# Performance work log

Measured on AMD Instinct MI355X. Metric: run time of the kernel, lower is better.

## Reference

```python
import jax, jax.numpy as jnp
import numpy as np

NEG_INF = -100000000.0  # matches masked_fill value in torch source

def setup_inputs() -> dict:
    key = jax.random.key(0)
    ks = jax.random.split(key, 7)
    d_model, d = 1024, 128
    B, S = 4, 2048
    scale = 1.0 / np.sqrt(d_model)
    x = jax.random.normal(ks[0], (B, S, d_model), dtype=jnp.float32)
    Wq = jax.random.normal(ks[1], (d, d_model), dtype=jnp.float32) * scale
    bq = jax.random.normal(ks[2], (d,), dtype=jnp.float32) * 0.02
    Wk = jax.random.normal(ks[3], (d, d_model), dtype=jnp.float32) * scale
    bk = jax.random.normal(ks[4], (d,), dtype=jnp.float32) * 0.02
    Wv = jax.random.normal(ks[5], (d, d_model), dtype=jnp.float32) * scale
    bv = jax.random.normal(ks[6], (d,), dtype=jnp.float32) * 0.02
    return {"x": x, "Wq": Wq, "bq": bq, "Wk": Wk, "bk": bk, "Wv": Wv, "bv": bv}

def reference(x, Wq, bq, Wk, bk, Wv, bv):
    # Q,K,V: [B,S,d] via torch Linear (x @ W.T + b)
    Q = jnp.einsum('bsm,dm->bsd', x, Wq) + bq
    K = jnp.einsum('bsm,dm->bsd', x, Wk) + bk
    V = jnp.einsum('bsm,dm->bsd', x, Wv) + bv
    d = Wk.shape[0]
    scale = 1.0 / jnp.sqrt(jnp.asarray(d, dtype=Q.dtype))
    scores = jnp.einsum('bqd,bkd->bqk', Q, K) * scale  # [B,S,S]
    # Faithful to source: tril then value-based mask (tril==0 -> -1e8).
    tril = jnp.tril(scores)
    masked = jnp.where(tril == 0, NEG_INF, tril)
    attn = jax.nn.softmax(masked, axis=-1)
    context = jnp.einsum('bqk,bkd->bqd', attn, V)
    return context
```

## Files before the change

### kernel.cpp

```cpp
#include <hip/hip_runtime.h>

typedef __attribute__((ext_vector_type(8))) short bf16x8;
typedef __attribute__((ext_vector_type(4))) float f32x4;

__device__ __forceinline__ unsigned short f2bf(float f) {
    unsigned int u = __float_as_uint(f);
    u += 0x7fffu + ((u >> 16) & 1u);
    return (unsigned short)(u >> 16);
}
__device__ __forceinline__ unsigned int pack2bf(float lo, float hi) {
    return (unsigned int)f2bf(lo) | ((unsigned int)f2bf(hi) << 16);
}
__device__ __forceinline__ void async_ld16(void* lds, const void* g) {
    __builtin_amdgcn_global_load_lds(
        (const __attribute__((address_space(1))) unsigned int*)g,
        (__attribute__((address_space(3))) unsigned int*)lds, 16, 0, 0);
}

__global__ __launch_bounds__(256) void conv_w(
    const float* __restrict__ Wq, const float* __restrict__ Wk,
    const float* __restrict__ Wv, unsigned short* __restrict__ Wcat)
{
    size_t o = ((size_t)blockIdx.x * 256 + threadIdx.x) * 8;
    int sel = (int)(o >> 17);
    const float* W = (sel == 0) ? Wq : ((sel == 1) ? Wk : Wv);
    const float* src = W + (o & 131071);
    float4 f0 = ((const float4*)src)[0];
    float4 f1 = ((const float4*)src)[1];
    uint4 u;
    u.x = pack2bf(f0.x, f0.y); u.y = pack2bf(f0.z, f0.w);
    u.z = pack2bf(f1.x, f1.y); u.w = pack2bf(f1.z, f1.w);
    *(uint4*)(Wcat + o) = u;
}

__global__ __launch_bounds__(256) void qkv_gemm(
    const float* __restrict__ x,
    const unsigned short* __restrict__ Wcat,
    const float* __restrict__ bq, const float* __restrict__ bk,
    const float* __restrict__ bv,
    unsigned short* __restrict__ Qg,
    unsigned short* __restrict__ Kg,
    unsigned short* __restrict__ Vtg)
{
    __shared__ unsigned short As[2][32 * 64];
    __shared__ unsigned short Bs[2][128 * 64];

    const int tid  = threadIdx.x;
    const int lane = tid & 63;
    const int w    = tid >> 6;
    const int quad = lane >> 4;
    const int ln   = lane & 15;
    const int lr   = lane >> 3;
    const int csw  = ((lane & 7) ^ lr) * 8;

    const int bid   = blockIdx.x;
    const int nb    = bid >> 8;
    const int mbase = (bid & 255) * 32;
    const unsigned short* Wsel = Wcat + (size_t)nb * 128 * 1024;

    const int arow  = tid >> 3;
    const int achk  = tid & 7;
    const int aslot = achk ^ (arow & 7);
    const float* xsrc = x + (size_t)(mbase + arow) * 1024 + achk * 8;
    unsigned short* adst0 = &As[0][arow * 64 + aslot * 8];
    unsigned short* adst1 = &As[1][arow * 64 + aslot * 8];

    f32x4 acc[2][2];
#pragma unroll
    for (int mt = 0; mt < 2; mt++)
#pragma unroll
        for (int nt = 0; nt < 2; nt++) acc[mt][nt] = (f32x4){0.f, 0.f, 0.f, 0.f};

    auto stageB = [&](int kb, int p) {
        const int kcol = kb * 64 + csw;
#pragma unroll
        for (int j = 0; j < 4; j++) {
            int chunk = w * 4 + j;
            async_ld16(&Bs[p][chunk * 512 + lane * 8],
                       Wsel + (size_t)(chunk * 8 + lr) * 1024 + kcol);
        }
    };
    auto writeA = [&](int p, const float4& f0, const float4& f1) {
        uint4 u;
        u.x = pack2bf(f0.x, f0.y); u.y = pack2bf(f0.z, f0.w);
        u.z = pack2bf(f1.x, f1.y); u.w = pack2bf(f1.z, f1.w);
        *(uint4*)((p == 0) ? adst0 : adst1) = u;
    };

    float4 a0 = ((const float4*)xsrc)[0];
    float4 a1 = ((const float4*)xsrc)[1];
    stageB(0, 0);
    writeA(0, a0, a1);
    __syncthreads();

    for (int kb = 0; kb < 16; kb++) {
        const int p = kb & 1;
        float4 n0, n1;
        if (kb < 15) {
            stageB(kb + 1, p ^ 1);
            const float* xs = xsrc + (kb + 1) * 64;
            n0 = ((const float4*)xs)[0];
            n1 = ((const float4*)xs)[1];
        }
#pragma unroll
        for (int ks = 0; ks < 2; ks++) {
            bf16x8 a[2], b[2];
#pragma unroll
            for (int mt = 0; mt < 2; mt++) {
                int row = mt * 16 + ln;
                a[mt] = *(const bf16x8*)&As[p][row * 64 + ((ks * 4 + quad) ^ (ln & 7)) * 8];
            }
#pragma unroll
            for (int nt = 0; nt < 2; nt++) {
                int row = w * 32 + nt * 16 + ln;
                b[nt] = *(const bf16x8*)&Bs[p][row * 64 + ((ks * 4 + quad) ^ (ln & 7)) * 8];
            }
#pragma unroll
            for (int mt = 0; mt < 2; mt++)
#pragma unroll
                for (int nt = 0; nt < 2; nt++)
                    acc[mt][nt] = __builtin_amdgcn_mfma_f32_16x16x32_bf16(
                        a[mt], b[nt], acc[mt][nt], 0, 0, 0);
        }
        if (kb < 15) writeA(p ^ 1, n0, n1);
        __syncthreads();
    }

    const float scale = (nb == 0) ? 0.08838834764831845f : 1.0f;
    const float* bsel = (nb == 0) ? bq : ((nb == 1) ? bk : bv);
    float bias_v[2];
#pragma unroll
    for (int nt = 0; nt < 2; nt++) bias_v[nt] = bsel[w * 32 + nt * 16 + ln];

    if (nb < 2) {
        unsigned short* dst = (nb == 0) ? Qg : Kg;
#pragma unroll
        for (int mt = 0; mt < 2; mt++)
#pragma unroll
            for (int nt = 0; nt < 2; nt++)
#pragma unroll
                for (int r = 0; r < 4; r++) {
                    int m = mbase + mt * 16 + quad * 4 + r;
                    int d = w * 32 + nt * 16 + ln;
                    dst[(size_t)m * 128 + d] =
                        f2bf((acc[mt][nt][r] + bias_v[nt]) * scale);
                }
    } else {
#pragma unroll
        for (int mt = 0; mt < 2; mt++)
#pragma unroll
            for (int nt = 0; nt < 2; nt++) {
                int dd = w * 32 + nt * 16 + ln;
                int m0 = mbase + mt * 16 + quad * 4;
                int bb = m0 >> 11, s0 = m0 & 2047;
                ushort4 u = { f2bf(acc[mt][nt][0] + bias_v[nt]),
                              f2bf(acc[mt][nt][1] + bias_v[nt]),
                              f2bf(acc[mt][nt][2] + bias_v[nt]),
                              f2bf(acc[mt][nt][3] + bias_v[nt]) };
                *(ushort4*)&Vtg[((size_t)bb * 128 + dd) * 2048 + s0] = u;
            }
    }
}

__global__ __launch_bounds__(256) void flash_attn(
    const unsigned short* __restrict__ Qg,
    const unsigned short* __restrict__ Kg,
    const unsigned short* __restrict__ Vtg,
    unsigned short* __restrict__ Opart,
    float2* __restrict__ ml)
{
    __shared__ unsigned short Ks[2][64 * 128];
    __shared__ unsigned short Vts[2][128 * 64];
    __shared__ unsigned short Pl[64][72];

    const int b = blockIdx.x;
    const int q = blockIdx.y;
    const int c = blockIdx.z;
    if (c > (q >> 2)) return;

    const int m4 = q >> 2, r4 = q & 3;
    const int pidx = b * 144 + q + 2 * m4 * (m4 - 1) + r4 * m4 + c;
    const int k0 = c * 4;
    const int kend = (c * 4 + 4 < q + 1) ? (c * 4 + 4) : (q + 1);

    const int tid  = threadIdx.x;
    const int lane = tid & 63, w = tid >> 6, quad = lane >> 4, ln = lane & 15;

    bf16x8 qa[4];
    const unsigned short* qrow =
        Qg + ((size_t)b * 2048 + q * 64 + w * 16 + ln) * 128 + quad * 8;
#pragma unroll
    for (int ks = 0; ks < 4; ks++) qa[ks] = *(const bf16x8*)(qrow + ks * 32);

    auto stage = [&](int kt, int p) {
        const unsigned short* ksrc = Kg + ((size_t)b * 2048 + kt * 64) * 128;
        const int krl = lane >> 4;
#pragma unroll
        for (int j = 0; j < 4; j++) {
            int chunk = w * 4 + j;
            int row = chunk * 4 + krl;
            int cd = (lane & 15) ^ (row & 15);
            async_ld16(&Ks[p][chunk * 512 + lane * 8],
                       ksrc + (size_t)row * 128 + cd * 8);
        }
        const unsigned short* vsrc = Vtg + (size_t)b * 128 * 2048 + kt * 64;
        const int vrl = lane >> 3;
#pragma unroll
        for (int j = 0; j < 4; j++) {
            int chunk = w * 4 + j;
            int row = chunk * 8 + vrl;
            int cd = (lane & 7) ^ (row & 7);
            async_ld16(&Vts[p][chunk * 512 + lane * 8],
                       vsrc + (size_t)row * 2048 + cd * 8);
        }
    };

    float m_i[4], l_i[4];
    f32x4 Ofr[8];
#pragma unroll
    for (int r = 0; r < 4; r++) { m_i[r] = -__builtin_inff(); l_i[r] = 0.f; }
#pragma unroll
    for (int dt = 0; dt < 8; dt++) Ofr[dt] = (f32x4){0.f, 0.f, 0.f, 0.f};

    stage(k0, 0);
    __syncthreads();

    int p = 0;
    for (int kt = k0; kt < kend; kt++) {
        if (kt + 1 < kend) stage(kt + 1, p ^ 1);

        f32x4 sfr[4];
#pragma unroll
        for (int ct = 0; ct < 4; ct++) {
            f32x4 s = (f32x4){0.f, 0.f, 0.f, 0.f};
#pragma unroll
            for (int ks = 0; ks < 4; ks++) {
                int row = ct * 16 + ln;
                bf16x8 kf = *(const bf16x8*)&Ks[p][row * 128 + ((ks * 4 + quad) ^ ln) * 8];
                s = __builtin_amdgcn_mfma_f32_16x16x32_bf16(qa[ks], kf, s, 0, 0, 0);
            }
            sfr[ct] = s;
        }

        if (kt == q) {
#pragma unroll
            for (int ct = 0; ct < 4; ct++)
#pragma unroll
                for (int r = 0; r < 4; r++)
                    if (ct * 16 + ln > w * 16 + quad * 4 + r)
                        sfr[ct][r] = -__builtin_inff();
        }

        float mrow[4];
#pragma unroll
        for (int r = 0; r < 4; r++) mrow[r] = -__builtin_inff();
#pragma unroll
        for (int ct = 0; ct < 4; ct++)
#pragma unroll
            for (int r = 0; r < 4; r++) mrow[r] = fmaxf(mrow[r], sfr[ct][r]);
#pragma unroll
        for (int off = 1; off < 16; off <<= 1)
#pragma unroll
            for (int r = 0; r < 4; r++)
                mrow[r] = fmaxf(mrow[r], __shfl_xor(mrow[r], off, 64));

        float alpha[4], rs[4];
#pragma unroll
        for (int r = 0; r < 4; r++) {
            float mn = fmaxf(m_i[r], mrow[r]);
            alpha[r] = __expf(m_i[r] - mn);
            m_i[r]   = mn;
            rs[r]    = 0.f;
        }
#pragma unroll
        for (int ct = 0; ct < 4; ct++)
#pragma unroll
            for (int r = 0; r < 4; r++) {
                float pv = __expf(sfr[ct][r] - m_i[r]);
                rs[r] += pv;
                Pl[w * 16 + quad * 4 + r][ct * 16 + ln] = f2bf(pv);
            }
#pragma unroll
        for (int off = 1; off < 16; off <<= 1)
#pragma unroll
            for (int r = 0; r < 4; r++) rs[r] += __shfl_xor(rs[r], off, 64);
#pragma unroll
        for (int r = 0; r < 4; r++) l_i[r] = l_i[r] * alpha[r] + rs[r];
#pragma unroll
        for (int dt = 0; dt < 8; dt++)
#pragma unroll
            for (int r = 0; r < 4; r++) Ofr[dt][r] *= alpha[r];

        __syncthreads();

#pragma unroll
        for (int kstep = 0; kstep < 2; kstep++) {
            bf16x8 pa = *(const bf16x8*)&Pl[w * 16 + ln][kstep * 32 + quad * 8];
#pragma unroll
            for (int dt = 0; dt < 8; dt++) {
                int row = dt * 16 + ln;
                bf16x8 vf = *(const bf16x8*)&Vts[p][row * 64 + ((kstep * 4 + quad) ^ (ln & 7)) * 8];
                Ofr[dt] = __builtin_amdgcn_mfma_f32_16x16x32_bf16(pa, vf, Ofr[dt], 0, 0, 0);
            }
        }
        __syncthreads();
        p ^= 1;
    }

#pragma unroll
    for (int dt = 0; dt < 8; dt++)
#pragma unroll
        for (int r = 0; r < 4; r++) {
            int row = w * 16 + quad * 4 + r;
            Opart[((size_t)pidx * 64 + row) * 128 + dt * 16 + ln] = f2bf(Ofr[dt][r]);
        }
    if (ln == 0) {
#pragma unroll
        for (int r = 0; r < 4; r++) {
            int row = w * 16 + quad * 4 + r;
            ml[(size_t)pidx * 64 + row] = make_float2(m_i[r], l_i[r]);
        }
    }
}

__global__ __launch_bounds__(256) void combine(
    const unsigned short* __restrict__ Opart,
    const float2* __restrict__ ml,
    float* __restrict__ out)
{
    const int idx  = blockIdx.x >> 1;
    const int half = blockIdx.x & 1;
    const int b = idx >> 5, q = idx & 31;
    const int m4 = q >> 2, r4 = q & 3;
    const int pbase = b * 144 + q + 2 * m4 * (m4 - 1) + r4 * m4;
    const int nc = m4 + 1;

    const int row = threadIdx.x & 63;
    const int grp = half * 64 + (threadIdx.x >> 6) * 16;

    float2 t[8];
#pragma unroll
    for (int c2 = 0; c2 < 8; c2++) {
        int cc = (c2 < nc) ? c2 : (nc - 1);
        t[c2] = ml[(size_t)(pbase + cc) * 64 + row];
    }
    float mc[8], lc[8], wgt[8];
    float mmax = -__builtin_inff();
#pragma unroll
    for (int c2 = 0; c2 < 8; c2++) {
        mc[c2] = (c2 < nc) ? t[c2].x : -__builtin_inff();
        lc[c2] = (c2 < nc) ? t[c2].y : 0.f;
        mmax = fmaxf(mmax, mc[c2]);
    }
    float lsum = 0.f;
#pragma unroll
    for (int c2 = 0; c2 < 8; c2++) {
        wgt[c2] = __expf(mc[c2] - mmax);
        lsum += lc[c2] * wgt[c2];
    }
    const float inv = 1.0f / lsum;

#pragma unroll
    for (int v = 0; v < 2; v++) {
        int col = grp + v * 8;
        float acc[8];
#pragma unroll
        for (int k = 0; k < 8; k++) acc[k] = 0.f;
#pragma unroll
        for (int c2 = 0; c2 < 8; c2++) {
            int cc = (c2 < nc) ? c2 : (nc - 1);
            uint4 u = *(const uint4*)&Opart[((size_t)(pbase + cc) * 64 + row) * 128 + col];
            float wc = wgt[c2];
            acc[0] += wc * __uint_as_float(u.x << 16);
            acc[1] += wc * __uint_as_float(u.x & 0xffff0000u);
            acc[2] += wc * __uint_as_float(u.y << 16);
            acc[3] += wc * __uint_as_float(u.y & 0xffff0000u);
            acc[4] += wc * __uint_as_float(u.z << 16);
            acc[5] += wc * __uint_as_float(u.z & 0xffff0000u);
            acc[6] += wc * __uint_as_float(u.w << 16);
            acc[7] += wc * __uint_as_float(u.w & 0xffff0000u);
        }
        float* o = &out[((size_t)b * 2048 + q * 64 + row) * 128 + col];
        float4 o0 = { acc[0] * inv, acc[1] * inv, acc[2] * inv, acc[3] * inv };
        float4 o1 = { acc[4] * inv, acc[5] * inv, acc[6] * inv, acc[7] * inv };
        ((float4*)o)[0] = o0;
        ((float4*)o)[1] = o1;
    }
}

extern "C" void kernel_launch(void* const* d_in, const int* in_sizes, int n_in,
                              void* d_out, int out_size, void* d_ws, size_t ws_size,
                              hipStream_t stream) {
    const float* x  = (const float*)d_in[0];
    const float* Wq = (const float*)d_in[1];
    const float* bq = (const float*)d_in[2];
    const float* Wk = (const float*)d_in[3];
    const float* bk = (const float*)d_in[4];
    const float* Wv = (const float*)d_in[5];
    const float* bv = (const float*)d_in[6];
    float* out = (float*)d_out;

    char* wsb = (char*)d_ws;
    unsigned short* Opart = (unsigned short*)wsb;
    float2*         ml    = (float2*)(wsb + 9437184);
    unsigned short* Wcat  = (unsigned short*)(wsb + 10485760);
    unsigned short* Qg    = (unsigned short*)(wsb + 11272192);
    unsigned short* Kg    = Qg + (size_t)8192 * 128;
    unsigned short* Vtg   = Qg + (size_t)2 * 8192 * 128;

    conv_w<<<192, 256, 0, stream>>>(Wq, Wk, Wv, Wcat);
    qkv_gemm<<<768, 256, 0, stream>>>(x, Wcat, bq, bk, bv, Qg, Kg, Vtg);
    flash_attn<<<dim3(4, 32, 8), 256, 0, stream>>>(Qg, Kg, Vtg, Opart, ml);
    combine<<<256, 256, 0, stream>>>(Opart, ml, out);
}
```

Baseline: 129.1 us.

## Fuse split-K combine into flash attention via last-block atomic counter

Removes the separate combine kernel. Each attention block now bumps a per-(batch, query-tile) atomic counter after writing its partial output, and the block that arrives last merges all partials and writes the final fp32 output. The counters are zeroed inside conv_w. It also drops the __syncthreads between writing P to LDS and reading it back, because each wave only reads its own rows. This saves a kernel launch and its tail, at the cost of fences, an atomic per block, and serial combine work on the last-arriving block.

Result: slower. 215.8 us (+67.2%).

```diff
diff --git a/kernel.cpp b/kernel.cpp
--- a/kernel.cpp
+++ b/kernel.cpp
@@ -19,8 +19,10 @@
 
 __global__ __launch_bounds__(256) void conv_w(
     const float* __restrict__ Wq, const float* __restrict__ Wk,
-    const float* __restrict__ Wv, unsigned short* __restrict__ Wcat)
+    const float* __restrict__ Wv, unsigned short* __restrict__ Wcat,
+    unsigned int* __restrict__ counters)
 {
+    if (blockIdx.x == 0 && threadIdx.x < 128) counters[threadIdx.x] = 0u;
     size_t o = ((size_t)blockIdx.x * 256 + threadIdx.x) * 8;
     int sel = (int)(o >> 17);
     const float* W = (sel == 0) ? Wq : ((sel == 1) ? Wk : Wv);
@@ -167,19 +169,23 @@
     const unsigned short* __restrict__ Kg,
     const unsigned short* __restrict__ Vtg,
     unsigned short* __restrict__ Opart,
-    float2* __restrict__ ml)
+    float2* __restrict__ ml,
+    unsigned int* __restrict__ counters,
+    float* __restrict__ out)
 {
     __shared__ unsigned short Ks[2][64 * 128];
     __shared__ unsigned short Vts[2][128 * 64];
     __shared__ unsigned short Pl[64][72];
+    __shared__ unsigned int lastflag;
 
     const int b = blockIdx.x;
     const int q = blockIdx.y;
     const int c = blockIdx.z;
-    if (c > (q >> 2)) return;
-
     const int m4 = q >> 2, r4 = q & 3;
-    const int pidx = b * 144 + q + 2 * m4 * (m4 - 1) + r4 * m4 + c;
+    if (c > m4) return;
+
+    const int pbase = b * 144 + q + 2 * m4 * (m4 - 1) + r4 * m4;
+    const int pidx  = pbase + c;
     const int k0 = c * 4;
     const int kend = (c * 4 + 4 < q + 1) ? (c * 4 + 4) : (q + 1);
 
@@ -291,8 +297,6 @@
 #pragma unroll
             for (int r = 0; r < 4; r++) Ofr[dt][r] *= alpha[r];
 
-        __syncthreads();
-
 #pragma unroll
         for (int kstep = 0; kstep < 2; kstep++) {
             bf16x8 pa = *(const bf16x8*)&Pl[w * 16 + ln][kstep * 32 + quad * 8];
@@ -321,22 +325,20 @@
             ml[(size_t)pidx * 64 + row] = make_float2(m_i[r], l_i[r]);
         }
     }
-}
-
-__global__ __launch_bounds__(256) void combine(
-    const unsigned short* __restrict__ Opart,
-    const float2* __restrict__ ml,
-    float* __restrict__ out)
-{
-    const int idx  = blockIdx.x >> 1;
-    const int half = blockIdx.x & 1;
-    const int b = idx >> 5, q = idx & 31;
-    const int m4 = q >> 2, r4 = q & 3;
-    const int pbase = b * 144 + q + 2 * m4 * (m4 - 1) + r4 * m4;
-    const int nc = m4 + 1;
-
-    const int row = threadIdx.x & 63;
-    const int grp = half * 64 + (threadIdx.x >> 6) * 16;
+
+    __threadfence();
+    __syncthreads();
+    if (tid == 0) {
+        unsigned int old = atomicAdd(&counters[b * 32 + q], 1u);
+        lastflag = (old == (unsigned int)m4);
+    }
+    __syncthreads();
+    if (!lastflag) return;
+    __threadfence();
+
+    const int nc  = m4 + 1;
+    const int row = tid & 63;
+    const int grp = (tid >> 6) * 32;
 
     float2 t[8];
 #pragma unroll
@@ -344,45 +346,45 @@
         int cc = (c2 < nc) ? c2 : (nc - 1);
         t[c2] = ml[(size_t)(pbase + cc) * 64 + row];
     }
-    float mc[8], lc[8], wgt[8];
+    float mc[8], lc2[8], wgt[8];
     float mmax = -__builtin_inff();
 #pragma unroll
     for (int c2 = 0; c2 < 8; c2++) {
-        mc[c2] = (c2 < nc) ? t[c2].x : -__builtin_inff();
-        lc[c2] = (c2 < nc) ? t[c2].y : 0.f;
+        mc[c2]  = (c2 < nc) ? t[c2].x : -__builtin_inff();
+        lc2[c2] = (c2 < nc) ? t[c2].y : 0.f;
         mmax = fmaxf(mmax, mc[c2]);
     }
     float lsum = 0.f;
 #pragma unroll
     for (int c2 = 0; c2 < 8; c2++) {
         wgt[c2] = __expf(mc[c2] - mmax);
-        lsum += lc[c2] * wgt[c2];
+        lsum += lc2[c2] * wgt[c2];
     }
     const float inv = 1.0f / lsum;
 
 #pragma unroll
-    for (int v = 0; v < 2; v++) {
+    for (int v = 0; v < 4; v++) {
         int col = grp + v * 8;
-        float acc[8];
-#pragma unroll
-        for (int k = 0; k < 8; k++) acc[k] = 0.f;
+        float acc2[8];
+#pragma unroll
+        for (int k = 0; k < 8; k++) acc2[k] = 0.f;
 #pragma unroll
         for (int c2 = 0; c2 < 8; c2++) {
             int cc = (c2 < nc) ? c2 : (nc - 1);
             uint4 u = *(const uint4*)&Opart[((size_t)(pbase + cc) * 64 + row) * 128 + col];
             float wc = wgt[c2];
-            acc[0] += wc * __uint_as_float(u.x << 16);
-            acc[1] += wc * __uint_as_float(u.x & 0xffff0000u);
-            acc[2] += wc * __uint_as_float(u.y << 16);
-            acc[3] += wc * __uint_as_float(u.y & 0xffff0000u);
-            acc[4] += wc * __uint_as_float(u.z << 16);
-            acc[5] += wc * __uint_as_float(u.z & 0xffff0000u);
-            acc[6] += wc * __uint_as_float(u.w << 16);
-            acc[7] += wc * __uint_as_float(u.w & 0xffff0000u);
+            acc2[0] += wc * __uint_as_float(u.x << 16);
+            acc2[1] += wc * __uint_as_float(u.x & 0xffff0000u);
+            acc2[2] += wc * __uint_as_float(u.y << 16);
+            acc2[3] += wc * __uint_as_float(u.y & 0xffff0000u);
+            acc2[4] += wc * __uint_as_float(u.z << 16);
+            acc2[5] += wc * __uint_as_float(u.z & 0xffff0000u);
+            acc2[6] += wc * __uint_as_float(u.w << 16);
+            acc2[7] += wc * __uint_as_float(u.w & 0xffff0000u);
         }
         float* o = &out[((size_t)b * 2048 + q * 64 + row) * 128 + col];
-        float4 o0 = { acc[0] * inv, acc[1] * inv, acc[2] * inv, acc[3] * inv };
-        float4 o1 = { acc[4] * inv, acc[5] * inv, acc[6] * inv, acc[7] * inv };
+        float4 o0 = { acc2[0] * inv, acc2[1] * inv, acc2[2] * inv, acc2[3] * inv };
+        float4 o1 = { acc2[4] * inv, acc2[5] * inv, acc2[6] * inv, acc2[7] * inv };
         ((float4*)o)[0] = o0;
         ((float4*)o)[1] = o1;
     }
@@ -403,13 +405,13 @@
     char* wsb = (char*)d_ws;
     unsigned short* Opart = (unsigned short*)wsb;
     float2*         ml    = (float2*)(wsb + 9437184);
+    unsigned int*   ctr   = (unsigned int*)(wsb + 9732096);
     unsigned short* Wcat  = (unsigned short*)(wsb + 10485760);
     unsigned short* Qg    = (unsigned short*)(wsb + 11272192);
     unsigned short* Kg    = Qg + (size_t)8192 * 128;
     unsigned short* Vtg   = Qg + (size_t)2 * 8192 * 128;
 
-    conv_w<<<192, 256, 0, stream>>>(Wq, Wk, Wv, Wcat);
+    conv_w<<<192, 256, 0, stream>>>(Wq, Wk, Wv, Wcat, ctr);
     qkv_gemm<<<768, 256, 0, stream>>>(x, Wcat, bq, bk, bv, Qg, Kg, Vtg);
-    flash_attn<<<dim3(4, 32, 8), 256, 0, stream>>>(Qg, Kg, Vtg, Opart, ml);
-    combine<<<256, 256, 0, stream>>>(Opart, ml, out);
-}
+    flash_attn<<<dim3(4, 32, 8), 256, 0, stream>>>(Qg, Kg, Vtg, Opart, ml, ctr, out);
+}
```
